# Performance work log

Hardware: AMD Instinct MI355X
Metric: run time of the kernel (lower is better)

## Reference

```python
import jax, jax.numpy as jnp
import numpy as np

NUM_HEADS = 8
KEY_DIM = 32
ATTN_RATIO = 4
RESOLUTION = 7
VAL_DIM = KEY_DIM * ATTN_RATIO  # 128
SCALE = KEY_DIM ** (-0.5)


def _bias_idxs():
    # (2, N) grid positions, N = resolution^2
    r = RESOLUTION
    gh, gw = np.meshgrid(np.arange(r), np.arange(r), indexing='ij')
    pos = np.stack([gh, gw], 0).reshape(2, -1)
    rel = np.abs(pos[:, :, None] - pos[:, None, :])
    return jnp.asarray(rel[0] * r + rel[1], dtype=jnp.int32)  # (N, N)


def setup_inputs() -> dict:
    key = jax.random.key(0)
    ks = jax.random.split(key, 4)
    B, N, D = 2048, RESOLUTION * RESOLUTION, 384
    qkv_out = KEY_DIM * NUM_HEADS * 2 + VAL_DIM * NUM_HEADS  # 1536
    return {
        'x': jax.random.normal(ks[0], (B, N, D), jnp.float32),
        'qkv_kernel': jax.random.normal(ks[1], (D, qkv_out), jnp.float32) * 0.02,
        'qkv_bias': jnp.zeros((qkv_out,), jnp.float32),
        'proj_kernel': jax.random.normal(ks[2], (VAL_DIM * NUM_HEADS, D), jnp.float32) * 0.02,
        'proj_bias': jnp.zeros((D,), jnp.float32),
        'attention_biases': jax.random.normal(ks[3], (NUM_HEADS, N), jnp.float32) * 0.02,
    }


def reference(x, qkv_kernel, qkv_bias, proj_kernel, proj_bias, attention_biases):
    B, N, _ = x.shape
    idxs = _bias_idxs()  # (N, N) int32
    qkv = jnp.matmul(x, qkv_kernel) + qkv_bias            # (B, N, 1536)
    qkv = qkv.reshape(B, N, NUM_HEADS, -1).transpose(0, 2, 1, 3)  # (B, H, N, 2k+v)
    q = qkv[..., :KEY_DIM]
    k = qkv[..., KEY_DIM:2 * KEY_DIM]
    v = qkv[..., 2 * KEY_DIM:]
    attn = jnp.einsum('bhnd,bhmd->bhnm', q, k) * SCALE    # (B, H, N, N)
    bias = attention_biases[:, idxs]                       # (H, N, N) gather
    attn = jax.nn.softmax(attn + bias, axis=-1)
    out = jnp.einsum('bhnm,bhmd->bhnd', attn, v)           # (B, H, N, val_dim)
    out = out.transpose(0, 2, 1, 3).reshape(B, N, NUM_HEADS * VAL_DIM)
    return jnp.matmul(out, proj_kernel) + proj_bias
```

## Files before the change

kernel.cpp:

```cpp
#include <hip/hip_runtime.h>
#include <hip/hip_bf16.h>

using bf16x8 = short __attribute__((ext_vector_type(8)));
using f32x16 = float __attribute__((ext_vector_type(16)));

#define MROWS 100352
#define SCALE_Q 0.17677669529663687f

static __device__ __forceinline__ unsigned short f2bs(float f){
  unsigned u = __builtin_bit_cast(unsigned, f);
  unsigned r = (u + 0x7FFFu + ((u >> 16) & 1u)) >> 16;
  return (unsigned short)r;
}
static __device__ __forceinline__ unsigned packbf(float a, float b){
  return (unsigned)f2bs(a) | ((unsigned)f2bs(b) << 16);
}

__global__ void k_xcast(const float* __restrict__ x, short* __restrict__ xb){
  const int i = blockIdx.x*256 + threadIdx.x;
  const float4 u0 = *reinterpret_cast<const float4*>(x + (size_t)i*8);
  const float4 u1 = *reinterpret_cast<const float4*>(x + (size_t)i*8 + 4);
  bf16x8 t;
  t[0]=(short)f2bs(u0.x); t[1]=(short)f2bs(u0.y); t[2]=(short)f2bs(u0.z); t[3]=(short)f2bs(u0.w);
  t[4]=(short)f2bs(u1.x); t[5]=(short)f2bs(u1.y); t[6]=(short)f2bs(u1.z); t[7]=(short)f2bs(u1.w);
  *reinterpret_cast<bf16x8*>(xb + (size_t)i*8) = t;
}

__global__ void k_convert(const float* __restrict__ qkvW, const float* __restrict__ qkvB,
                          const float* __restrict__ projW, const float* __restrict__ ab,
                          short* __restrict__ WqkvT, short* __restrict__ WpT,
                          float* __restrict__ bqkv, float* __restrict__ bias_exp){
  int i = blockIdx.x*256 + threadIdx.x;
  if (i < 1536*384){
    int c = i/384, f = i - c*384;
    int src; float sc = 1.0f;
    if (c < 512){ src = (c>>6)*192 + (c&63); if ((c&63) < 32) sc = SCALE_Q; }
    else        { int dv = c - 512; src = (dv>>7)*192 + 64 + (dv&127); }
    WqkvT[i] = (short)f2bs(qkvW[f*1536 + src] * sc);
    return;
  }
  i -= 1536*384;
  if (i < 384*1024){
    int j = i/1024, m = i - j*1024;
    WpT[i] = (short)f2bs(projW[m*384 + j]);
    return;
  }
  i -= 384*1024;
  if (i < 1536){
    int c = i; int src; float sc = 1.0f;
    if (c < 512){ src = (c>>6)*192 + (c&63); if ((c&63) < 32) sc = SCALE_Q; }
    else        { int dv = c - 512; src = (dv>>7)*192 + 64 + (dv&127); }
    bqkv[c] = qkvB[src] * sc;
    return;
  }
  i -= 1536;
  if (i < 8*64*49){
    int h = i / (64*49), rem = i - h*(64*49);
    int r = rem / 49, n = rem - r*49;
    float v = 0.0f;
    if (r < 49){
      int rh = r/7, rw = r - rh*7, ch = n/7, cw = n - ch*7;
      int dh = rh>ch?rh-ch:ch-rh, dw = rw>cw?rw-cw:cw-rw;
      v = ab[h*49 + dh*7 + dw];
    }
    bias_exp[i] = v;
  }
}

template<int KTOT, int NT, int NSLAB, bool F32OUT>
__global__ __launch_bounds__(512) void k_gemm(const short* __restrict__ A,
                                              const short* __restrict__ Bw,
                                              const float* __restrict__ bias,
                                              void* __restrict__ Cout, int ldc){
  constexpr int BN = NT*128;
  __shared__ short Alds[128*64];
  __shared__ short Blds[BN*64];
  const int lane = threadIdx.x & 63, w = threadIdx.x >> 6;
  const int hi = lane >> 5, l31 = lane & 31;
  const int wm = w >> 2, wn = w & 3;

  const int nwg = NSLAB * 784;
  const int lin = blockIdx.x + NSLAB * blockIdx.y;
  const int swz = (lin & 7) * (nwg >> 3) + (lin >> 3);
  const int slab = swz % NSLAB, panel = swz / NSLAB;
  const size_t R0 = (size_t)panel * 128, C0 = (size_t)slab * BN;

  f32x16 acc[2][NT];
  #pragma unroll
  for (int mt=0; mt<2; ++mt)
    #pragma unroll
    for (int nt=0; nt<NT; ++nt) acc[mt][nt] = (f32x16)0.0f;

  const int srow = lane >> 3;
  const int sG   = ((lane & 7) ^ srow) * 8;
  const short* aG = A  + (R0 + (size_t)(w*8 + srow))*KTOT + sG;
  const short* bG = Bw + (C0 + (size_t)(w*8 + srow))*KTOT + sG;

  constexpr int NK = KTOT/64;
  for (int kt=0; kt<NK; ++kt){
    #pragma unroll
    for (int j=0; j<2; ++j)
      __builtin_amdgcn_global_load_lds(
        (const unsigned int __attribute__((address_space(1)))*)(aG + (size_t)j*64*KTOT + kt*64),
        (unsigned int __attribute__((address_space(3)))*)(&Alds[(j*64 + w*8)*64]), 16, 0, 0);
    #pragma unroll
    for (int j=0; j<2*NT; ++j)
      __builtin_amdgcn_global_load_lds(
        (const unsigned int __attribute__((address_space(1)))*)(bG + (size_t)j*64*KTOT + kt*64),
        (unsigned int __attribute__((address_space(3)))*)(&Blds[(j*64 + w*8)*64]), 16, 0, 0);
    __syncthreads();
    #pragma unroll
    for (int ks=0; ks<4; ++ks){
      bf16x8 aF[2], bF[NT];
      #pragma unroll
      for (int mt=0; mt<2; ++mt){
        const int rA = wm*64 + mt*32 + l31;
        aF[mt] = *reinterpret_cast<const bf16x8*>(
                   (const char*)Alds + rA*128 + ((((ks<<1)|hi) ^ (rA&7))<<4));
      }
      #pragma unroll
      for (int nt=0; nt<NT; ++nt){
        const int rB = wn*(NT*32) + nt*32 + l31;
        bF[nt] = *reinterpret_cast<const bf16x8*>(
                   (const char*)Blds + rB*128 + ((((ks<<1)|hi) ^ (rB&7))<<4));
      }
      #pragma unroll
      for (int mt=0; mt<2; ++mt)
        #pragma unroll
        for (int nt=0; nt<NT; ++nt)
          acc[mt][nt] = __builtin_amdgcn_mfma_f32_32x32x16_bf16(aF[mt], bF[nt], acc[mt][nt], 0,0,0);
    }
    __syncthreads();
  }

  #pragma unroll
  for (int nt=0; nt<NT; ++nt){
    const int c = (int)C0 + wn*(NT*32) + nt*32 + l31;
    const float bb = bias[c];
    #pragma unroll
    for (int mt=0; mt<2; ++mt){
      const size_t rbase = R0 + wm*64 + mt*32;
      #pragma unroll
      for (int rg=0; rg<16; ++rg){
        const size_t r = rbase + (rg&3) + 8*(rg>>2) + 4*hi;
        if constexpr (F32OUT) ((float*)Cout)[r*ldc + c] = acc[mt][nt][rg] + bb;
        else                  ((short*)Cout)[r*ldc + c] = (short)f2bs(acc[mt][nt][rg] + bb);
      }
    }
  }
}

__global__ __launch_bounds__(256) void k_attn(const short* __restrict__ qkvbuf,
                                              const float* __restrict__ bias_exp, short* __restrict__ aout){
  const int lane = threadIdx.x & 63, w = threadIdx.x >> 6;
  const int hi = lane >> 5, l31 = lane & 31;
  const int b = blockIdx.x, hg = blockIdx.y;
  const int h = hg*4 + w;

  __shared__ short vlds[4*49*136];

  for (int i=0; i<13; ++i){
    const int n = i*4 + w;
    if (n < 49){
      const bf16x8 vv = *reinterpret_cast<const bf16x8*>(qkvbuf + (b*49+n)*1536 + 512 + hg*512 + lane*8);
      const int hh = lane >> 4;
      const int d0 = ((lane & 15) * 8) ^ (((n>>3)&1) << 5);
      *reinterpret_cast<bf16x8*>(&vlds[(hh*49 + n)*136 + d0]) = vv;
    }
  }
  __syncthreads();

  bf16x8 kf[2][2];
  #pragma unroll
  for (int mt=0; mt<2; ++mt){
    const int n = 32*mt + l31;
    #pragma unroll
    for (int ks=0; ks<2; ++ks)
      kf[mt][ks] = (n < 49)
        ? *reinterpret_cast<const bf16x8*>(qkvbuf + (b*49+n)*1536 + h*64 + 32 + ks*16 + hi*8)
        : (bf16x8)(short)0;
  }
  const short* vb = &vlds[w*49*136];
  const int dxbase = hi << 5;

  for (int rb=0; rb<2; ++rb){
    const int r = 32*rb + l31;
    bf16x8 qf[2];
    #pragma unroll
    for (int ks=0; ks<2; ++ks)
      qf[ks] = (r < 49)
        ? *reinterpret_cast<const bf16x8*>(qkvbuf + (b*49+r)*1536 + h*64 + ks*16 + hi*8)
        : (bf16x8)(short)0;

    f32x16 s[2];
    s[0] = (f32x16)0.0f; s[1] = (f32x16)0.0f;
    #pragma unroll
    for (int ks=0; ks<2; ++ks){
      s[0] = __builtin_amdgcn_mfma_f32_32x32x16_bf16(kf[0][ks], qf[ks], s[0], 0, 0, 0);
      s[1] = __builtin_amdgcn_mfma_f32_32x32x16_bf16(kf[1][ks], qf[ks], s[1], 0, 0, 0);
    }

    float mloc = -3.0e38f;
    #pragma unroll
    for (int mt=0; mt<2; ++mt)
      #pragma unroll
      for (int rg=0; rg<16; ++rg){
        const int n = 32*mt + (rg&3) + 8*(rg>>2) + 4*hi;
        float v = s[mt][rg];
        v = (n < 49) ? v + bias_exp[(h*64 + r)*49 + n] : -1.0e30f;
        s[mt][rg] = v;
        mloc = fmaxf(mloc, v);
      }
    const float mrow = fmaxf(mloc, __shfl_xor(mloc, 32));
    float sloc = 0.0f;
    #pragma unroll
    for (int mt=0; mt<2; ++mt)
      #pragma unroll
      for (int rg=0; rg<16; ++rg){
        const float p = __expf(s[mt][rg] - mrow);
        s[mt][rg] = p; sloc += p;
      }
    const float inv = 1.0f / (sloc + __shfl_xor(sloc, 32));
    #pragma unroll
    for (int mt=0; mt<2; ++mt)
      #pragma unroll
      for (int rg=0; rg<16; ++rg) s[mt][rg] *= inv;

    unsigned pk[8][2];
    #pragma unroll
    for (int o=0; o<8; ++o){
      const int mt = o>>2, base = 4*(o&3);
      pk[o][0] = packbf(s[mt][base+0], s[mt][base+1]);
      pk[o][1] = packbf(s[mt][base+2], s[mt][base+3]);
    }
    bf16x8 af[4];
    #pragma unroll
    for (int ks=0; ks<4; ++ks){
      const unsigned e0 = pk[2*ks][0],   e1 = pk[2*ks][1];
      const unsigned o0 = pk[2*ks+1][0], o1 = pk[2*ks+1][1];
      const unsigned own0 = hi ? o0 : e0, own1 = hi ? o1 : e1;
      const unsigned oth0 = hi ? e0 : o0, oth1 = hi ? e1 : o1;
      const unsigned sw0 = __shfl_xor(oth0, 32), sw1 = __shfl_xor(oth1, 32);
      const unsigned lo0 = hi ? sw0 : own0, lo1 = hi ? sw1 : own1;
      const unsigned h0  = hi ? own0 : sw0, h1  = hi ? own1 : sw1;
      union { bf16x8 v; unsigned u[4]; } t;
      t.u[0]=lo0; t.u[1]=lo1; t.u[2]=h0; t.u[3]=h1;
      af[ks] = t.v;
    }

    #pragma unroll
    for (int dt=0; dt<4; ++dt){
      const int dx = (dt*32 + l31) ^ dxbase;
      f32x16 acc = (f32x16)0.0f;
      #pragma unroll
      for (int ks=0; ks<4; ++ks){
        bf16x8 t;
        if (ks < 3){
          const int nb = ks*16 + hi*8;
          #pragma unroll
          for (int j=0; j<8; ++j) t[j] = vb[(nb + j)*136 + dx];
        } else {
          #pragma unroll
          for (int j=0; j<8; ++j) t[j] = 0;
          if (hi == 0) t[0] = vb[48*136 + (dt*32 + l31)];
        }
        acc = __builtin_amdgcn_mfma_f32_32x32x16_bf16(af[ks], t, acc, 0, 0, 0);
      }
      #pragma unroll
      for (int rg=0; rg<16; ++rg){
        const int rr = 32*rb + (rg&3) + 8*(rg>>2) + 4*hi;
        if (rr < 49)
          aout[(b*49+rr)*1024 + h*128 + dt*32 + l31] = (short)f2bs(acc[rg]);
      }
    }
  }
}

extern "C" void kernel_launch(void* const* d_in, const int* in_sizes, int n_in,
                              void* d_out, int out_size, void* d_ws, size_t ws_size,
                              hipStream_t stream) {
  const float* x     = (const float*)d_in[0];
  const float* qkvW  = (const float*)d_in[1];
  const float* qkvB  = (const float*)d_in[2];
  const float* projW = (const float*)d_in[3];
  const float* projB = (const float*)d_in[4];
  const float* ab    = (const float*)d_in[5];

  char* ws = (char*)d_ws;
  short* aoutb = (short*)ws;
  short* xb    = (short*)ws;
  size_t off = (size_t)MROWS*1024*2;
  short* qkvbuf = (short*)(ws + off); off += (size_t)MROWS*1536*2;
  short* WqkvT  = (short*)(ws + off); off += (size_t)1536*384*2;
  short* WpT    = (short*)(ws + off); off += (size_t)384*1024*2;
  float* bqkv   = (float*)(ws + off); off += (size_t)1536*4;
  float* bias_exp = (float*)(ws + off); off += (size_t)8*64*49*4;
  if (ws_size < off) return;

  const int conv_total = 1536*384 + 384*1024 + 1536 + 8*64*49;
  k_convert<<<(conv_total + 255)/256, 256, 0, stream>>>(qkvW, qkvB, projW, ab,
                                                        WqkvT, WpT, bqkv, bias_exp);
  k_xcast<<<MROWS*384/8/256, 256, 0, stream>>>(x, xb);
  k_gemm<384, 2, 6, false><<<dim3(6, 784), 512, 0, stream>>>(xb, WqkvT, bqkv, qkvbuf, 1536);
  k_attn<<<dim3(2048, 2), 256, 0, stream>>>(qkvbuf, bias_exp, aoutb);
  k_gemm<1024, 3, 1, true><<<dim3(1, 784), 512, 0, stream>>>(aoutb, WpT, projB, d_out, 384);
}
```

Baseline: 547.5 us.

## Fuse attention with output projection GEMM in one per-batch kernel

Merges the attention kernel and the projection GEMM into a single kernel with one block per batch item and eight waves, one per head. The attention output stays in LDS as bf16 and is multiplied directly by the projection weights, so the intermediate no longer makes a round trip through HBM. In exchange, each block re-reads the full projection weight matrix straight from global memory (hopefully served from L2), uses a large LDS buffer that limits occupancy, and runs the projection on only 49 rows padded to 64.

```diff
diff --git a/kernel.cpp b/kernel.cpp
--- a/kernel.cpp
+++ b/kernel.cpp
@@ -150,25 +150,35 @@
   }
 }
 
-__global__ __launch_bounds__(256) void k_attn(const short* __restrict__ qkvbuf,
-                                              const float* __restrict__ bias_exp, short* __restrict__ aout){
-  const int lane = threadIdx.x & 63, w = threadIdx.x >> 6;
+__global__ __launch_bounds__(512) void k_attnproj(const short* __restrict__ qkvbuf,
+                                                  const float* __restrict__ bias_exp,
+                                                  const short* __restrict__ WpT,
+                                                  const float* __restrict__ pb,
+                                                  float* __restrict__ out){
+  const int t = threadIdx.x;
+  const int lane = t & 63, w = t >> 6;
   const int hi = lane >> 5, l31 = lane & 31;
-  const int b = blockIdx.x, hg = blockIdx.y;
-  const int h = hg*4 + w;
-
-  __shared__ short vlds[4*49*136];
-
-  for (int i=0; i<13; ++i){
-    const int n = i*4 + w;
-    if (n < 49){
-      const bf16x8 vv = *reinterpret_cast<const bf16x8*>(qkvbuf + (b*49+n)*1536 + 512 + hg*512 + lane*8);
-      const int hh = lane >> 4;
-      const int d0 = ((lane & 15) * 8) ^ (((n>>3)&1) << 5);
-      *reinterpret_cast<bf16x8*>(&vlds[(hh*49 + n)*136 + d0]) = vv;
-    }
-  }
-  __syncthreads();
+  const int b = blockIdx.x;
+  const int h = w;
+
+  __shared__ short lds[8*49*136];
+
+  {
+    const int nidx = t >> 7;
+    const int within = t & 127;
+    const int hh = within >> 4;
+    const int d0 = ((within & 15) * 8) ^ (((0)&1) << 5);
+    #pragma unroll
+    for (int i=0; i<13; ++i){
+      const int n = i*4 + nidx;
+      if (n < 49){
+        const bf16x8 vv = *reinterpret_cast<const bf16x8*>(qkvbuf + (b*49+n)*1536 + 512 + within*8);
+        const int dd = ((within & 15) * 8) ^ (((n>>3)&1) << 5);
+        *reinterpret_cast<bf16x8*>(&lds[(hh*49 + n)*136 + dd]) = vv;
+      }
+    }
+    (void)d0;
+  }
 
   bf16x8 kf[2][2];
   #pragma unroll
@@ -180,8 +190,11 @@
         ? *reinterpret_cast<const bf16x8*>(qkvbuf + (b*49+n)*1536 + h*64 + 32 + ks*16 + hi*8)
         : (bf16x8)(short)0;
   }
-  const short* vb = &vlds[w*49*136];
+  __syncthreads();
+
+  const short* vb = &lds[h*49*136];
   const int dxbase = hi << 5;
+  unsigned pko[2][4][8];
 
   for (int rb=0; rb<2; ++rb){
     const int r = 32*rb + l31;
@@ -243,9 +256,9 @@
       const unsigned sw0 = __shfl_xor(oth0, 32), sw1 = __shfl_xor(oth1, 32);
       const unsigned lo0 = hi ? sw0 : own0, lo1 = hi ? sw1 : own1;
       const unsigned h0  = hi ? own0 : sw0, h1  = hi ? own1 : sw1;
-      union { bf16x8 v; unsigned u[4]; } t;
-      t.u[0]=lo0; t.u[1]=lo1; t.u[2]=h0; t.u[3]=h1;
-      af[ks] = t.v;
+      union { bf16x8 v; unsigned u[4]; } tt;
+      tt.u[0]=lo0; tt.u[1]=lo1; tt.u[2]=h0; tt.u[3]=h1;
+      af[ks] = tt.v;
     }
 
     #pragma unroll
@@ -254,23 +267,63 @@
       f32x16 acc = (f32x16)0.0f;
       #pragma unroll
       for (int ks=0; ks<4; ++ks){
-        bf16x8 t;
+        bf16x8 tt;
         if (ks < 3){
           const int nb = ks*16 + hi*8;
           #pragma unroll
-          for (int j=0; j<8; ++j) t[j] = vb[(nb + j)*136 + dx];
+          for (int j=0; j<8; ++j) tt[j] = vb[(nb + j)*136 + dx];
         } else {
           #pragma unroll
-          for (int j=0; j<8; ++j) t[j] = 0;
-          if (hi == 0) t[0] = vb[48*136 + (dt*32 + l31)];
+          for (int j=0; j<8; ++j) tt[j] = 0;
+          if (hi == 0) tt[0] = vb[48*136 + (dt*32 + l31)];
         }
-        acc = __builtin_amdgcn_mfma_f32_32x32x16_bf16(af[ks], t, acc, 0, 0, 0);
-      }
+        acc = __builtin_amdgcn_mfma_f32_32x32x16_bf16(af[ks], tt, acc, 0, 0, 0);
+      }
+      #pragma unroll
+      for (int j=0; j<8; ++j)
+        pko[rb][dt][j] = packbf(acc[2*j], acc[2*j+1]);
+    }
+  }
+  __syncthreads();
+
+  #pragma unroll
+  for (int rb=0; rb<2; ++rb)
+    #pragma unroll
+    for (int dt=0; dt<4; ++dt){
+      const int dcol = h*128 + dt*32 + l31;
+      #pragma unroll
+      for (int j=0; j<8; ++j){
+        const unsigned u = pko[rb][dt][j];
+        const int row0 = 32*rb + ((2*j)&3) + 8*(j>>1) + 4*hi;
+        if (row0 < 49)   lds[row0*1032 + dcol] = (short)(u & 0xFFFFu);
+        if (row0+1 < 49) lds[(row0+1)*1032 + dcol] = (short)(u >> 16);
+      }
+    }
+  __syncthreads();
+
+  {
+    const int wm = w >> 2, wn = w & 3;
+    const int rA = (wm*32 + l31 > 48) ? 48 : (wm*32 + l31);
+    f32x16 acc[3];
+    acc[0]=(f32x16)0.0f; acc[1]=(f32x16)0.0f; acc[2]=(f32x16)0.0f;
+    for (int ks=0; ks<64; ++ks){
+      const bf16x8 aF = *reinterpret_cast<const bf16x8*>(&lds[rA*1032 + ks*16 + hi*8]);
+      #pragma unroll
+      for (int nt=0; nt<3; ++nt){
+        const int c = wn*96 + nt*32 + l31;
+        const bf16x8 bF = *reinterpret_cast<const bf16x8*>(WpT + c*1024 + ks*16 + hi*8);
+        acc[nt] = __builtin_amdgcn_mfma_f32_32x32x16_bf16(aF, bF, acc[nt], 0, 0, 0);
+      }
+    }
+    #pragma unroll
+    for (int nt=0; nt<3; ++nt){
+      const int c = wn*96 + nt*32 + l31;
+      const float bb = pb[c];
       #pragma unroll
       for (int rg=0; rg<16; ++rg){
-        const int rr = 32*rb + (rg&3) + 8*(rg>>2) + 4*hi;
-        if (rr < 49)
-          aout[(b*49+rr)*1024 + h*128 + dt*32 + l31] = (short)f2bs(acc[rg]);
+        const int r = wm*32 + (rg&3) + 8*(rg>>2) + 4*hi;
+        if (r < 49)
+          out[((size_t)b*49 + r)*384 + c] = acc[nt][rg] + bb;
       }
     }
   }
@@ -287,7 +340,6 @@
   const float* ab    = (const float*)d_in[5];
 
   char* ws = (char*)d_ws;
-  short* aoutb = (short*)ws;
   short* xb    = (short*)ws;
   size_t off = (size_t)MROWS*1024*2;
   short* qkvbuf = (short*)(ws + off); off += (size_t)MROWS*1536*2;
@@ -302,6 +354,5 @@
                                                         WqkvT, WpT, bqkv, bias_exp);
   k_xcast<<<MROWS*384/8/256, 256, 0, stream>>>(x, xb);
   k_gemm<384, 2, 6, false><<<dim3(6, 784), 512, 0, stream>>>(xb, WqkvT, bqkv, qkvbuf, 1536);
-  k_attn<<<dim3(2048, 2), 256, 0, stream>>>(qkvbuf, bias_exp, aoutb);
-  k_gemm<1024, 3, 1, true><<<dim3(1, 784), 512, 0, stream>>>(aoutb, WpT, projB, d_out, 384);
-}
+  k_attnproj<<<2048, 512, 0, stream>>>(qkvbuf, bias_exp, WpT, projB, (float*)d_out);
+}
```

New measurement: 745.9 us. 36.2% more time.

## Replace projection GEMM with smaller-tile kernel using direct global-to-LDS loads

Applied to the files above, without the earlier changes.

Swaps the output projection GEMM from the generic 512-thread kernel (one block per 128-row panel covering all 384 columns) to a dedicated 256-thread kernel with 128x128 tiles, giving three times as many workgroups. It uses global_load_lds to stream A and B tiles straight into XOR-swizzled shared memory, and a swizzled block ordering for cache locality. This aims to improve occupancy and load balance for the K=1024 projection. The new kernel has no double buffering and synchronizes twice per K step, so load latency may not be hidden, and A panels are re-read once per column slab.

```diff
diff --git a/kernel.cpp b/kernel.cpp
--- a/kernel.cpp
+++ b/kernel.cpp
@@ -150,6 +150,81 @@
   }
 }
 
+__global__ __launch_bounds__(256) void k_proj4(const short* __restrict__ A,
+                                               const short* __restrict__ Bw,
+                                               const float* __restrict__ bias,
+                                               float* __restrict__ out){
+  __shared__ short Alds[128*64];
+  __shared__ short Blds[128*64];
+  const int lane = threadIdx.x & 63, w = threadIdx.x >> 6;
+  const int hi = lane >> 5, l31 = lane & 31;
+  const int wm = w >> 1, wn = w & 1;
+
+  const int nwg = 3 * 784;
+  const int lin = blockIdx.x + 3 * blockIdx.y;
+  const int swz = (lin & 7) * (nwg >> 3) + (lin >> 3);
+  const int slab = swz % 3, panel = swz / 3;
+  const size_t R0 = (size_t)panel * 128, C0 = (size_t)slab * 128;
+
+  f32x16 acc[2][2];
+  acc[0][0]=(f32x16)0.f; acc[0][1]=(f32x16)0.f; acc[1][0]=(f32x16)0.f; acc[1][1]=(f32x16)0.f;
+
+  const int srow = lane >> 3;
+  const int sG   = ((lane & 7) ^ srow) * 8;
+  const short* aG = A  + (R0 + (size_t)(w*8 + srow))*1024 + sG;
+  const short* bG = Bw + (C0 + (size_t)(w*8 + srow))*1024 + sG;
+
+  for (int kt=0; kt<16; ++kt){
+    #pragma unroll
+    for (int j=0; j<4; ++j){
+      __builtin_amdgcn_global_load_lds(
+        (const unsigned int __attribute__((address_space(1)))*)(aG + (size_t)j*32*1024 + kt*64),
+        (unsigned int __attribute__((address_space(3)))*)(&Alds[(j*32 + w*8)*64]), 16, 0, 0);
+      __builtin_amdgcn_global_load_lds(
+        (const unsigned int __attribute__((address_space(1)))*)(bG + (size_t)j*32*1024 + kt*64),
+        (unsigned int __attribute__((address_space(3)))*)(&Blds[(j*32 + w*8)*64]), 16, 0, 0);
+    }
+    __syncthreads();
+    #pragma unroll
+    for (int ks=0; ks<4; ++ks){
+      bf16x8 aF[2], bF[2];
+      #pragma unroll
+      for (int mt=0; mt<2; ++mt){
+        const int rA = wm*64 + mt*32 + l31;
+        aF[mt] = *reinterpret_cast<const bf16x8*>(
+                   (const char*)Alds + rA*128 + ((((ks<<1)|hi) ^ (rA&7))<<4));
+      }
+      #pragma unroll
+      for (int nt=0; nt<2; ++nt){
+        const int rB = wn*64 + nt*32 + l31;
+        bF[nt] = *reinterpret_cast<const bf16x8*>(
+                   (const char*)Blds + rB*128 + ((((ks<<1)|hi) ^ (rB&7))<<4));
+      }
+      #pragma unroll
+      for (int mt=0; mt<2; ++mt)
+        #pragma unroll
+        for (int nt=0; nt<2; ++nt)
+          acc[mt][nt] = __builtin_amdgcn_mfma_f32_32x32x16_bf16(aF[mt], bF[nt], acc[mt][nt], 0,0,0);
+    }
+    __syncthreads();
+  }
+
+  #pragma unroll
+  for (int nt=0; nt<2; ++nt){
+    const int c = (int)C0 + wn*64 + nt*32 + l31;
+    const float bb = bias[c];
+    #pragma unroll
+    for (int mt=0; mt<2; ++mt){
+      const size_t rbase = R0 + wm*64 + mt*32;
+      #pragma unroll
+      for (int rg=0; rg<16; ++rg){
+        const size_t r = rbase + (rg&3) + 8*(rg>>2) + 4*hi;
+        out[r*384 + c] = acc[mt][nt][rg] + bb;
+      }
+    }
+  }
+}
+
 __global__ __launch_bounds__(256) void k_attn(const short* __restrict__ qkvbuf,
                                               const float* __restrict__ bias_exp, short* __restrict__ aout){
   const int lane = threadIdx.x & 63, w = threadIdx.x >> 6;
@@ -303,5 +378,5 @@
   k_xcast<<<MROWS*384/8/256, 256, 0, stream>>>(x, xb);
   k_gemm<384, 2, 6, false><<<dim3(6, 784), 512, 0, stream>>>(xb, WqkvT, bqkv, qkvbuf, 1536);
   k_attn<<<dim3(2048, 2), 256, 0, stream>>>(qkvbuf, bias_exp, aoutb);
-  k_gemm<1024, 3, 1, true><<<dim3(1, 784), 512, 0, stream>>>(aoutb, WpT, projB, d_out, 384);
-}
+  k_proj4<<<dim3(3, 784), 256, 0, stream>>>(aoutb, WpT, projB, (float*)d_out);
+}
```

New measurement: 499.0 us. 1.1x faster.
